# Performance work log

Hardware: AMD Instinct MI355X
Metric: run time of the kernel (lower is better)

The kernel has to match this reference:

```python
import jax, jax.numpy as jnp
from jax import lax
import numpy as np

DIM, RESO, HEADS, SPLIT, B = 128, 112, 4, 7, 2
HID = 4 * DIM  # mlp_ratio=4


def _ln(x, g, b):
    m = x.mean(-1, keepdims=True)
    v = ((x - m) ** 2).mean(-1, keepdims=True)
    return (x - m) * lax.rsqrt(v + 1e-5) * g + b


def _lepe_attn(q, k, v, cw, cb, H, W, H_sp, W_sp, nh):
    # q,k,v: [B, H*W, C] (C = branch dim); cw: depthwise conv weight [C,1,3,3]
    Bq, L, C = q.shape
    hd = C // nh
    scale = hd ** -0.5
    nHw, nWw = H // H_sp, W // W_sp

    def to_win(t):  # [B,H,W,C] -> [B*nHw*nWw, nh, H_sp*W_sp, hd]
        t = t.reshape(Bq, nHw, H_sp, nWw, W_sp, C).transpose(0, 1, 3, 2, 4, 5)
        return t.reshape(-1, H_sp * W_sp, nh, hd).transpose(0, 2, 1, 3)

    qw = to_win(q.reshape(Bq, H, W, C)) * scale
    kw = to_win(k.reshape(Bq, H, W, C))

    # v path: window partition in NCHW, depthwise conv LePE per window
    vimg = v.transpose(0, 2, 1).reshape(Bq, C, H, W)
    vimg = vimg.reshape(Bq, C, nHw, H_sp, nWw, W_sp).transpose(0, 2, 4, 1, 3, 5)
    vimg = vimg.reshape(-1, C, H_sp, W_sp)  # [B', C, H_sp, W_sp]
    lepe = lax.conv_general_dilated(vimg, cw, (1, 1), 'SAME', feature_group_count=C,
                                    dimension_numbers=('NCHW', 'OIHW', 'NCHW'))
    lepe = lepe + cb[None, :, None, None]
    vw = vimg.reshape(-1, nh, hd, H_sp * W_sp).transpose(0, 1, 3, 2)
    lepe = lepe.reshape(-1, nh, hd, H_sp * W_sp).transpose(0, 1, 3, 2)

    attn = jax.nn.softmax(jnp.einsum('whnd,whmd->whnm', qw, kw), axis=-1)
    o = jnp.einsum('whnm,whmd->whnd', attn, vw) + lepe  # [B', nh, S, hd]

    # windows2img
    o = o.transpose(0, 2, 1, 3).reshape(-1, H_sp * W_sp, C)
    o = o.reshape(Bq, nHw, nWw, H_sp, W_sp, C).transpose(0, 1, 3, 2, 4, 5)
    return o.reshape(Bq, H * W, C)


def setup_inputs() -> dict:
    key = jax.random.key(0)
    ks = jax.random.split(key, 16)
    s = 0.02
    Cb = DIM // 2
    return {
        'x': jax.random.normal(ks[0], (B, RESO * RESO, DIM), jnp.float32),
        'g1': jnp.ones((DIM,), jnp.float32),
        'b1': jnp.zeros((DIM,), jnp.float32),
        'w_qkv': s * jax.random.normal(ks[1], (3 * DIM, DIM), jnp.float32),
        'conv_w0': s * jax.random.normal(ks[2], (Cb, 1, 3, 3), jnp.float32),
        'conv_b0': jnp.zeros((Cb,), jnp.float32),
        'conv_w1': s * jax.random.normal(ks[3], (Cb, 1, 3, 3), jnp.float32),
        'conv_b1': jnp.zeros((Cb,), jnp.float32),
        'w_proj': s * jax.random.normal(ks[4], (DIM, DIM), jnp.float32),
        'b_proj': jnp.zeros((DIM,), jnp.float32),
        'g2': jnp.ones((DIM,), jnp.float32),
        'b2': jnp.zeros((DIM,), jnp.float32),
        'w_fc1': s * jax.random.normal(ks[5], (HID, DIM), jnp.float32),
        'b_fc1': jnp.zeros((HID,), jnp.float32),
        'w_fc2': s * jax.random.normal(ks[6], (DIM, HID), jnp.float32),
        'b_fc2': jnp.zeros((DIM,), jnp.float32),
    }


def reference(x, g1, b1, w_qkv, conv_w0, conv_b0, conv_w1, conv_b1,
              w_proj, b_proj, g2, b2, w_fc1, b_fc1, w_fc2, b_fc2):
    Bq, L, C = x.shape
    Cb = C // 2
    nh_b = HEADS // 2
    img = _ln(x, g1, b1)
    qkv = (img @ w_qkv.T).reshape(Bq, L, 3, C)  # qkv_bias=False
    q, k, v = qkv[:, :, 0], qkv[:, :, 1], qkv[:, :, 2]
    # branch 0: horizontal stripes (H_sp=RESO, W_sp=SPLIT) on first half of channels
    x1 = _lepe_attn(q[..., :Cb], k[..., :Cb], v[..., :Cb], conv_w0, conv_b0,
                    RESO, RESO, RESO, SPLIT, nh_b)
    # branch 1: vertical stripes (H_sp=SPLIT, W_sp=RESO) on second half
    x2 = _lepe_attn(q[..., Cb:], k[..., Cb:], v[..., Cb:], conv_w1, conv_b1,
                    RESO, RESO, SPLIT, RESO, nh_b)
    att = jnp.concatenate([x1, x2], axis=2)
    att = att @ w_proj.T + b_proj
    x = x + att  # drop_path = identity (prob 0)
    y = _ln(x, g2, b2)
    h = jax.nn.gelu(y @ w_fc1.T + b_fc1, approximate=False)
    x = x + (h @ w_fc2.T + b_fc2)
    return x
```

## Files before the change

kernel.cpp:

```cpp
#include <hip/hip_runtime.h>
#include <cstdint>

#define LTOK 12544
#define BATCH 2
#define CDIM 128
#define C3 384
#define RES 112
#define NROWS (BATCH * LTOK)
#define SCALE 0.17677669529663687f

typedef __attribute__((ext_vector_type(8))) short bf16x8;
typedef __attribute__((ext_vector_type(4))) float f32x4;

__device__ inline ushort f2b(float f) {
    union { float f; unsigned u; } v; v.f = f;
    unsigned r = (v.u + 0x7FFFu + ((v.u >> 16) & 1u)) >> 16;
    return (ushort)r;
}
__device__ inline float b2f(ushort u) {
    union { float f; unsigned u; } v; v.u = ((unsigned)u) << 16; return v.f;
}
__device__ inline float gelu_f(float a) {
    return 0.5f * a * (1.0f + erff(a * 0.70710678118654752f));
}

__device__ inline int ysIdx(int row, int el) { return row * 128 + (el ^ ((row & 7) << 3)); }
__device__ inline int hsIdx(int row, int el) { return row * 256 + (el ^ ((row & 7) << 3)); }
__device__ inline int xsIdx(int row, int el) { return row * 128 + (el ^ ((row & 7) << 2)); }

__device__ inline void nij(int n, int branch, int& i, int& j) {
    if (branch == 0) { i = n / 7; j = n - i * 7; }
    else             { i = n / 112; j = n - i * 112; }
}

__global__ __launch_bounds__(256) void k_cvt(const float* __restrict__ w0, const float* __restrict__ w1,
        const float* __restrict__ w2, const float* __restrict__ w3,
        ushort* __restrict__ o0, ushort* __restrict__ o1,
        ushort* __restrict__ o2, ushort* __restrict__ o3)
{
    int idx = blockIdx.x * 256 + threadIdx.x;
    const float* src; ushort* dst; int vi;
    if      (idx < 12288) { src = w0; dst = o0; vi = idx; }
    else if (idx < 16384) { src = w1; dst = o1; vi = idx - 12288; }
    else if (idx < 32768) { src = w2; dst = o2; vi = idx - 16384; }
    else                  { src = w3; dst = o3; vi = idx - 32768; }
    float4 v = ((const float4*)src)[vi];
    ushort4 r; r.x = f2b(v.x); r.y = f2b(v.y); r.z = f2b(v.z); r.w = f2b(v.w);
    ((ushort4*)dst)[vi] = r;
}

__global__ __launch_bounds__(256, 2) void k_ln_qkv(const float* __restrict__ x,
        const float* __restrict__ g1, const float* __restrict__ b1,
        const ushort* __restrict__ wqkv_bf, ushort* __restrict__ qkv)
{
    __shared__ ushort ys[32 * 128];
    const int tid = threadIdx.x;
    const long long row0 = (long long)blockIdx.x * 32;

    {
        const int r = tid >> 3, l8 = tid & 7;
        const float* xr = x + (row0 + r) * CDIM + l8 * 16;
        float4 a[4];
        #pragma unroll
        for (int i = 0; i < 4; ++i) a[i] = ((const float4*)xr)[i];
        float s = 0.f, s2 = 0.f;
        #pragma unroll
        for (int i = 0; i < 4; ++i) {
            s  += a[i].x + a[i].y + a[i].z + a[i].w;
            s2 += a[i].x*a[i].x + a[i].y*a[i].y + a[i].z*a[i].z + a[i].w*a[i].w;
        }
        #pragma unroll
        for (int m = 4; m >= 1; m >>= 1) { s += __shfl_xor(s, m, 8); s2 += __shfl_xor(s2, m, 8); }
        const float mean = s * (1.f / 128.f);
        const float var = s2 * (1.f / 128.f) - mean * mean;
        const float rs = rsqrtf(var + 1e-5f);
        #pragma unroll
        for (int i = 0; i < 4; ++i) {
            float4 gg = *(const float4*)(g1 + l8 * 16 + i * 4);
            float4 bb = *(const float4*)(b1 + l8 * 16 + i * 4);
            ushort4 w;
            w.x = f2b((a[i].x - mean) * rs * gg.x + bb.x);
            w.y = f2b((a[i].y - mean) * rs * gg.y + bb.y);
            w.z = f2b((a[i].z - mean) * rs * gg.z + bb.z);
            w.w = f2b((a[i].w - mean) * rs * gg.w + bb.w);
            *(ushort4*)&ys[ysIdx(r, l8 * 16 + i * 4)] = w;
        }
    }
    __syncthreads();

    const int wv = tid >> 6, lane = tid & 63;
    const int c16 = lane & 15, g = lane >> 4;

    bf16x8 yb[2][4];
    #pragma unroll
    for (int mt = 0; mt < 2; ++mt)
        #pragma unroll
        for (int kc = 0; kc < 4; ++kc)
            yb[mt][kc] = *(const bf16x8*)&ys[ysIdx(mt * 16 + c16, kc * 32 + g * 8)];

    bf16x8 wr[6][4];
    #pragma unroll
    for (int t = 0; t < 6; ++t)
        #pragma unroll
        for (int kc = 0; kc < 4; ++kc)
            wr[t][kc] = *(const bf16x8*)&wqkv_bf[(wv * 96 + t * 16 + c16) * CDIM + kc * 32 + g * 8];

    #pragma unroll
    for (int t = 0; t < 6; ++t) {
        const int n0 = wv * 96 + t * 16;
        #pragma unroll
        for (int mt = 0; mt < 2; ++mt) {
            f32x4 acc = {0.f, 0.f, 0.f, 0.f};
            #pragma unroll
            for (int kc = 0; kc < 4; ++kc)
                acc = __builtin_amdgcn_mfma_f32_16x16x32_bf16(wr[t][kc], yb[mt][kc], acc, 0, 0, 0);
            ushort4 sv;
            sv.x = f2b(acc[0]); sv.y = f2b(acc[1]); sv.z = f2b(acc[2]); sv.w = f2b(acc[3]);
            *(ushort4*)&qkv[(row0 + mt * 16 + c16) * C3 + n0 + g * 4] = sv;
        }
    }
}

__global__ __launch_bounds__(256) void k_attn_mfma(const ushort* __restrict__ qkv,
        const float* __restrict__ cw0, const float* __restrict__ cb0,
        const float* __restrict__ cw1, const float* __restrict__ cb1,
        ushort* __restrict__ att)
{
    __shared__ __align__(16) ushort ks[112 * 40];
    __shared__ __align__(16) ushort vt[32 * 136];
    __shared__ __align__(16) ushort pl[4][16 * 40];
    __shared__ __align__(16) float  ol[4][16 * 36];

    const int tid = threadIdx.x;
    const int wv = tid >> 6, lane = tid & 63;
    const int g = lane >> 4, c16 = lane & 15;

    const int wh = blockIdx.x;
    const int branch = wh >> 6;
    const int idx = wh & 63;
    const int win = idx >> 1, head = idx & 1;
    const int b = win >> 4, w = win & 15;
    const int rowBase = branch ? w * 7 : 0;
    const int colBase = branch ? 0 : w * 7;
    const float* cw = branch ? cw1 : cw0;
    const float* cb = branch ? cb1 : cb0;
    const int cbase = branch * 64 + head * 32;
    const long long qkvB = (long long)b * LTOK * C3;

    {
        const int row = tid >> 3, cwd = tid & 7;
        *(unsigned*)&vt[row * 136 + 112 + cwd * 2] = 0u;
    }

    const int t0 = blockIdx.y * 7 + 2 * wv;
    const int nt = (2 * wv + 1 < 7) ? 2 : 1;

    bf16x8 qf[2];
    #pragma unroll
    for (int t = 0; t < 2; ++t) if (t < nt) {
        int n = (t0 + t) * 16 + c16;
        int i, j; nij(n, branch, i, j);
        const ushort* qp = qkv + qkvB + (long long)((rowBase + i) * RES + colBase + j) * C3 + cbase + g * 8;
        bf16x8 qq = *(const bf16x8*)qp;
        #pragma unroll
        for (int e = 0; e < 8; ++e) qq[e] = (short)f2b(b2f((ushort)qq[e]) * SCALE);
        qf[t] = qq;
    }

    f32x4 O00 = {0.f,0.f,0.f,0.f}, O01 = {0.f,0.f,0.f,0.f};
    f32x4 O10 = {0.f,0.f,0.f,0.f}, O11 = {0.f,0.f,0.f,0.f};
    float lsum0[4] = {0.f,0.f,0.f,0.f};
    float lsum1[4] = {0.f,0.f,0.f,0.f};

    for (int cc = 0; cc < 7; ++cc) {
        __syncthreads();
        for (int u = tid; u < 448; u += 256) {
            const int key = u >> 2, d8 = (u & 3) * 8;
            const int n = cc * 112 + key;
            int i, j; nij(n, branch, i, j);
            const ushort* base = qkv + qkvB + (long long)((rowBase + i) * RES + colBase + j) * C3 + cbase + d8;
            bf16x8 kk = *(const bf16x8*)(base + 128);
            bf16x8 vv = *(const bf16x8*)(base + 256);
            *(bf16x8*)&ks[key * 40 + d8] = kk;
            #pragma unroll
            for (int e = 0; e < 8; ++e) vt[(d8 + e) * 136 + key] = (ushort)vv[e];
        }
        __syncthreads();

        #pragma unroll
        for (int p = 0; p < 4; ++p) {
            bf16x8 kf0 = *(const bf16x8*)&ks[(p * 32 + c16) * 40 + g * 8];
            bf16x8 kf1;
            if (p < 3) kf1 = *(const bf16x8*)&ks[(p * 32 + 16 + c16) * 40 + g * 8];
            bf16x8 vf0 = *(const bf16x8*)&vt[c16 * 136 + p * 32 + g * 8];
            bf16x8 vf1 = *(const bf16x8*)&vt[(16 + c16) * 136 + p * 32 + g * 8];
            ushort* pb = &pl[wv][0];

            #pragma unroll
            for (int t = 0; t < 2; ++t) if (t < nt) {
                const bf16x8 qq = t ? qf[1] : qf[0];
                f32x4 z = {0.f,0.f,0.f,0.f};
                f32x4 S0 = __builtin_amdgcn_mfma_f32_16x16x32_bf16(qq, kf0, z, 0, 0, 0);
                f32x4 S1 = z;
                if (p < 3) S1 = __builtin_amdgcn_mfma_f32_16x16x32_bf16(qq, kf1, z, 0, 0, 0);
                ushort pw0[4], pw1[4];
                #pragma unroll
                for (int r = 0; r < 4; ++r) {
                    float e0 = __expf(S0[r]);
                    if (t) lsum1[r] += e0; else lsum0[r] += e0;
                    pw0[r] = f2b(e0);
                    if (p < 3) {
                        float e1 = __expf(S1[r]);
                        if (t) lsum1[r] += e1; else lsum0[r] += e1;
                        pw1[r] = f2b(e1);
                    } else pw1[r] = 0;
                }
                #pragma unroll
                for (int r = 0; r < 4; ++r) {
                    pb[(g * 4 + r) * 40 + c16]      = pw0[r];
                    pb[(g * 4 + r) * 40 + 16 + c16] = pw1[r];
                }
                bf16x8 pf = *(const bf16x8*)&pb[c16 * 40 + g * 8];
                if (t) {
                    O10 = __builtin_amdgcn_mfma_f32_16x16x32_bf16(pf, vf0, O10, 0, 0, 0);
                    O11 = __builtin_amdgcn_mfma_f32_16x16x32_bf16(pf, vf1, O11, 0, 0, 0);
                } else {
                    O00 = __builtin_amdgcn_mfma_f32_16x16x32_bf16(pf, vf0, O00, 0, 0, 0);
                    O01 = __builtin_amdgcn_mfma_f32_16x16x32_bf16(pf, vf1, O01, 0, 0, 0);
                }
            }
        }
    }

    const int H_sp = branch ? 7 : RES;
    const int W_sp = branch ? RES : 7;
    #pragma unroll
    for (int t = 0; t < 2; ++t) if (t < nt) {
        float* ob = &ol[wv][0];
        #pragma unroll
        for (int r = 0; r < 4; ++r) {
            float s = t ? lsum1[r] : lsum0[r];
            s += __shfl_xor(s, 1); s += __shfl_xor(s, 2);
            s += __shfl_xor(s, 4); s += __shfl_xor(s, 8);
            const float inv = 1.f / s;
            const f32x4 Oa = t ? O10 : O00;
            const f32x4 Ob = t ? O11 : O01;
            ob[(g * 4 + r) * 36 + c16]      = Oa[r] * inv;
            ob[(g * 4 + r) * 36 + 16 + c16] = Ob[r] * inv;
        }
        const int r2 = lane >> 2, db = (lane & 3) * 8;
        const int n0 = (t0 + t) * 16 + r2;
        int i0, j0; nij(n0, branch, i0, j0);
        float acc[8];
        #pragma unroll
        for (int e = 0; e < 8; ++e) acc[e] = ob[r2 * 36 + db + e] + cb[head * 32 + db + e];
        #pragma unroll
        for (int dij = 0; dij < 9; ++dij) {
            const int di = dij / 3 - 1, dj = dij % 3 - 1;
            const int ii = i0 + di, jj = j0 + dj;
            if (ii >= 0 && ii < H_sp && jj >= 0 && jj < W_sp) {
                const ushort* vp = qkv + qkvB + (long long)((rowBase + ii) * RES + colBase + jj) * C3 + 256 + cbase + db;
                bf16x8 vv = *(const bf16x8*)vp;
                #pragma unroll
                for (int e = 0; e < 8; ++e)
                    acc[e] += cw[(head * 32 + db + e) * 9 + dij] * b2f((ushort)vv[e]);
            }
        }
        const long long Lq = (long long)(rowBase + i0) * RES + colBase + j0;
        ushort* op = att + ((long long)b * LTOK + Lq) * CDIM + cbase + db;
        bf16x8 ov;
        #pragma unroll
        for (int e = 0; e < 8; ++e) ov[e] = (short)f2b(acc[e]);
        *(bf16x8*)op = ov;
    }
}

__global__ __launch_bounds__(256, 2) void k_pmlp(const ushort* __restrict__ att,
        const ushort* __restrict__ wproj_bf, const float* __restrict__ bproj,
        const float* __restrict__ x,
        const float* __restrict__ g2, const float* __restrict__ b2,
        const ushort* __restrict__ w1bf, const float* __restrict__ bfc1,
        const ushort* __restrict__ w2bf, const float* __restrict__ bfc2,
        float* __restrict__ out)
{
    __shared__ union {
        float  xs[32 * 128];
        ushort hs[32 * 256];
    } u;
    __shared__ ushort ys[32 * 128];
    const int tid = threadIdx.x;
    const int wv = tid >> 6, lane = tid & 63;
    const int c16 = lane & 15, g = lane >> 4;
    const long long row0 = (long long)blockIdx.x * 32;

    f32x4 resid[2][2];
    {
        bf16x8 ab[2][4];
        #pragma unroll
        for (int mt = 0; mt < 2; ++mt)
            #pragma unroll
            for (int kc = 0; kc < 4; ++kc)
                ab[mt][kc] = *(const bf16x8*)&att[(row0 + mt * 16 + c16) * CDIM + kc * 32 + g * 8];

        bf16x8 awp[2][4];
        #pragma unroll
        for (int tt = 0; tt < 2; ++tt)
            #pragma unroll
            for (int kc = 0; kc < 4; ++kc)
                awp[tt][kc] = *(const bf16x8*)&wproj_bf[(wv * 32 + tt * 16 + c16) * CDIM + kc * 32 + g * 8];

        #pragma unroll
        for (int tt = 0; tt < 2; ++tt) {
            const int col = wv * 32 + tt * 16 + g * 4;
            float4 bb = *(const float4*)&bproj[col];
            #pragma unroll
            for (int mt = 0; mt < 2; ++mt) {
                f32x4 a = {0.f, 0.f, 0.f, 0.f};
                #pragma unroll
                for (int kc = 0; kc < 4; ++kc)
                    a = __builtin_amdgcn_mfma_f32_16x16x32_bf16(awp[tt][kc], ab[mt][kc], a, 0, 0, 0);
                float4 xv = *(const float4*)&x[(row0 + mt * 16 + c16) * CDIM + col];
                f32x4 r;
                r[0] = a[0] + xv.x + bb.x;
                r[1] = a[1] + xv.y + bb.y;
                r[2] = a[2] + xv.z + bb.z;
                r[3] = a[3] + xv.w + bb.w;
                resid[tt][mt] = r;
                *(float4*)&u.xs[xsIdx(mt * 16 + c16, col)] = make_float4(r[0], r[1], r[2], r[3]);
            }
        }
    }
    __syncthreads();

    {
        const int r = tid >> 3, l8 = tid & 7;
        float4 a[4];
        #pragma unroll
        for (int i = 0; i < 4; ++i) a[i] = *(const float4*)&u.xs[xsIdx(r, l8 * 16 + i * 4)];
        float s = 0.f, s2 = 0.f;
        #pragma unroll
        for (int i = 0; i < 4; ++i) {
            s  += a[i].x + a[i].y + a[i].z + a[i].w;
            s2 += a[i].x*a[i].x + a[i].y*a[i].y + a[i].z*a[i].z + a[i].w*a[i].w;
        }
        #pragma unroll
        for (int m = 4; m >= 1; m >>= 1) { s += __shfl_xor(s, m, 8); s2 += __shfl_xor(s2, m, 8); }
        const float mean = s * (1.f / 128.f);
        const float var = s2 * (1.f / 128.f) - mean * mean;
        const float rs = rsqrtf(var + 1e-5f);
        #pragma unroll
        for (int i = 0; i < 4; ++i) {
            float4 gg = *(const float4*)(g2 + l8 * 16 + i * 4);
            float4 bb = *(const float4*)(b2 + l8 * 16 + i * 4);
            ushort4 w;
            w.x = f2b((a[i].x - mean) * rs * gg.x + bb.x);
            w.y = f2b((a[i].y - mean) * rs * gg.y + bb.y);
            w.z = f2b((a[i].z - mean) * rs * gg.z + bb.z);
            w.w = f2b((a[i].w - mean) * rs * gg.w + bb.w);
            *(ushort4*)&ys[ysIdx(r, l8 * 16 + i * 4)] = w;
        }
    }
    __syncthreads();

    bf16x8 yb[2][4];
    #pragma unroll
    for (int mt = 0; mt < 2; ++mt)
        #pragma unroll
        for (int kc = 0; kc < 4; ++kc)
            yb[mt][kc] = *(const bf16x8*)&ys[ysIdx(mt * 16 + c16, kc * 32 + g * 8)];

    f32x4 acc2[2][2];
    #pragma unroll
    for (int tt = 0; tt < 2; ++tt)
        #pragma unroll
        for (int mt = 0; mt < 2; ++mt)
            acc2[tt][mt] = (f32x4){0.f, 0.f, 0.f, 0.f};

    #pragma unroll
    for (int half = 0; half < 2; ++half) {
        bf16x8 w1r[4][4];
        #pragma unroll
        for (int t = 0; t < 4; ++t)
            #pragma unroll
            for (int kc = 0; kc < 4; ++kc)
                w1r[t][kc] = *(const bf16x8*)&w1bf[(half * 256 + wv * 64 + t * 16 + c16) * CDIM + kc * 32 + g * 8];

        #pragma unroll
        for (int t = 0; t < 4; ++t) {
            const int n0g = half * 256 + wv * 64 + t * 16;
            float4 b1v = *(const float4*)&bfc1[n0g + g * 4];
            #pragma unroll
            for (int mt = 0; mt < 2; ++mt) {
                f32x4 a = {0.f, 0.f, 0.f, 0.f};
                #pragma unroll
                for (int kc = 0; kc < 4; ++kc)
                    a = __builtin_amdgcn_mfma_f32_16x16x32_bf16(w1r[t][kc], yb[mt][kc], a, 0, 0, 0);
                ushort4 sv;
                sv.x = f2b(gelu_f(a[0] + b1v.x));
                sv.y = f2b(gelu_f(a[1] + b1v.y));
                sv.z = f2b(gelu_f(a[2] + b1v.z));
                sv.w = f2b(gelu_f(a[3] + b1v.w));
                *(ushort4*)&u.hs[hsIdx(mt * 16 + c16, wv * 64 + t * 16 + g * 4)] = sv;
            }
        }

        bf16x8 w2r[2][8];
        #pragma unroll
        for (int tt = 0; tt < 2; ++tt)
            #pragma unroll
            for (int kc = 0; kc < 8; ++kc)
                w2r[tt][kc] = *(const bf16x8*)&w2bf[(wv * 32 + tt * 16 + c16) * 512 + half * 256 + kc * 32 + g * 8];

        __syncthreads();

        #pragma unroll
        for (int kc = 0; kc < 8; ++kc) {
            bf16x8 hb[2];
            #pragma unroll
            for (int mt = 0; mt < 2; ++mt)
                hb[mt] = *(const bf16x8*)&u.hs[hsIdx(mt * 16 + c16, kc * 32 + g * 8)];
            #pragma unroll
            for (int tt = 0; tt < 2; ++tt)
                #pragma unroll
                for (int mt = 0; mt < 2; ++mt)
                    acc2[tt][mt] = __builtin_amdgcn_mfma_f32_16x16x32_bf16(w2r[tt][kc], hb[mt], acc2[tt][mt], 0, 0, 0);
        }
        if (half == 0) __syncthreads();
    }

    #pragma unroll
    for (int tt = 0; tt < 2; ++tt) {
        const int col = wv * 32 + tt * 16 + g * 4;
        float4 bb = *(const float4*)&bfc2[col];
        #pragma unroll
        for (int mt = 0; mt < 2; ++mt) {
            const long long row = row0 + mt * 16 + c16;
            float4 o;
            o.x = acc2[tt][mt][0] + resid[tt][mt][0] + bb.x;
            o.y = acc2[tt][mt][1] + resid[tt][mt][1] + bb.y;
            o.z = acc2[tt][mt][2] + resid[tt][mt][2] + bb.z;
            o.w = acc2[tt][mt][3] + resid[tt][mt][3] + bb.w;
            *(float4*)&out[row * CDIM + col] = o;
        }
    }
}

extern "C" void kernel_launch(void* const* d_in, const int* in_sizes, int n_in,
                              void* d_out, int out_size, void* d_ws, size_t ws_size,
                              hipStream_t stream) {
    const float* x     = (const float*)d_in[0];
    const float* g1    = (const float*)d_in[1];
    const float* b1    = (const float*)d_in[2];
    const float* wqkv  = (const float*)d_in[3];
    const float* cw0   = (const float*)d_in[4];
    const float* cb0   = (const float*)d_in[5];
    const float* cw1   = (const float*)d_in[6];
    const float* cb1   = (const float*)d_in[7];
    const float* wproj = (const float*)d_in[8];
    const float* bproj = (const float*)d_in[9];
    const float* g2    = (const float*)d_in[10];
    const float* b2    = (const float*)d_in[11];
    const float* wfc1  = (const float*)d_in[12];
    const float* bfc1  = (const float*)d_in[13];
    const float* wfc2  = (const float*)d_in[14];
    const float* bfc2  = (const float*)d_in[15];

    char* wsb = (char*)d_ws;
    ushort* qkv_bf   = (ushort*)wsb;
    ushort* att_bf   = (ushort*)(wsb + 19267584);
    char*   wbase    = wsb + 19267584 + 6422528;
    ushort* wqkv_bf  = (ushort*)(wbase);
    ushort* wproj_bf = (ushort*)(wbase + 98304);
    ushort* wfc1_bf  = (ushort*)(wbase + 98304 + 32768);
    ushort* wfc2_bf  = (ushort*)(wbase + 98304 + 32768 + 131072);

    float* out = (float*)d_out;

    k_cvt<<<192, 256, 0, stream>>>(wqkv, wproj, wfc1, wfc2, wqkv_bf, wproj_bf, wfc1_bf, wfc2_bf);
    k_ln_qkv<<<NROWS / 32, 256, 0, stream>>>(x, g1, b1, wqkv_bf, qkv_bf);
    k_attn_mfma<<<dim3(128, 7), 256, 0, stream>>>(qkv_bf, cw0, cb0, cw1, cb1, att_bf);
    k_pmlp<<<NROWS / 32, 256, 0, stream>>>(att_bf, wproj_bf, bproj, x, g2, b2,
                                           wfc1_bf, bfc1, wfc2_bf, bfc2, out);
}
```

Before: 122.6 us.

## Double block size to 512 threads in LN-QKV and proj-MLP kernels

Both fused row-block kernels now run 8 waves per 32-row block instead of 4, so each wave owns half as many output columns. The LayerNorm stage uses 16 threads per row. The MLP kernel drops its two-pass split of the hidden dimension: the full 512-wide GELU hidden tile goes into shared memory and FC2 runs as a single K=512 pass. This raises parallelism per block and removes a sync round, but doubles LDS use for the hidden buffer and may lower blocks per CU and weight-register reuse per wave.

Result: slower. 135.7 us (+10.7%).

```diff
diff --git a/kernel.cpp b/kernel.cpp
--- a/kernel.cpp
+++ b/kernel.cpp
@@ -25,7 +25,7 @@
 }
 
 __device__ inline int ysIdx(int row, int el) { return row * 128 + (el ^ ((row & 7) << 3)); }
-__device__ inline int hsIdx(int row, int el) { return row * 256 + (el ^ ((row & 7) << 3)); }
+__device__ inline int hsIdx(int row, int el) { return row * 512 + (el ^ ((row & 7) << 3)); }
 __device__ inline int xsIdx(int row, int el) { return row * 128 + (el ^ ((row & 7) << 2)); }
 
 __device__ inline void nij(int n, int branch, int& i, int& j) {
@@ -49,7 +49,7 @@
     ((ushort4*)dst)[vi] = r;
 }
 
-__global__ __launch_bounds__(256, 2) void k_ln_qkv(const float* __restrict__ x,
+__global__ __launch_bounds__(512) void k_ln_qkv(const float* __restrict__ x,
         const float* __restrict__ g1, const float* __restrict__ b1,
         const ushort* __restrict__ wqkv_bf, ushort* __restrict__ qkv)
 {
@@ -58,33 +58,33 @@
     const long long row0 = (long long)blockIdx.x * 32;
 
     {
-        const int r = tid >> 3, l8 = tid & 7;
-        const float* xr = x + (row0 + r) * CDIM + l8 * 16;
-        float4 a[4];
-        #pragma unroll
-        for (int i = 0; i < 4; ++i) a[i] = ((const float4*)xr)[i];
-        float s = 0.f, s2 = 0.f;
-        #pragma unroll
-        for (int i = 0; i < 4; ++i) {
-            s  += a[i].x + a[i].y + a[i].z + a[i].w;
-            s2 += a[i].x*a[i].x + a[i].y*a[i].y + a[i].z*a[i].z + a[i].w*a[i].w;
-        }
-        #pragma unroll
-        for (int m = 4; m >= 1; m >>= 1) { s += __shfl_xor(s, m, 8); s2 += __shfl_xor(s2, m, 8); }
+        const int r = tid >> 4, l16 = tid & 15;
+        const float* xr = x + (row0 + r) * CDIM + l16 * 8;
+        float4 a0 = *(const float4*)xr;
+        float4 a1 = *(const float4*)(xr + 4);
+        float s  = a0.x + a0.y + a0.z + a0.w + a1.x + a1.y + a1.z + a1.w;
+        float s2 = a0.x*a0.x + a0.y*a0.y + a0.z*a0.z + a0.w*a0.w
+                 + a1.x*a1.x + a1.y*a1.y + a1.z*a1.z + a1.w*a1.w;
+        #pragma unroll
+        for (int m = 8; m >= 1; m >>= 1) { s += __shfl_xor(s, m, 16); s2 += __shfl_xor(s2, m, 16); }
         const float mean = s * (1.f / 128.f);
         const float var = s2 * (1.f / 128.f) - mean * mean;
         const float rs = rsqrtf(var + 1e-5f);
-        #pragma unroll
-        for (int i = 0; i < 4; ++i) {
-            float4 gg = *(const float4*)(g1 + l8 * 16 + i * 4);
-            float4 bb = *(const float4*)(b1 + l8 * 16 + i * 4);
-            ushort4 w;
-            w.x = f2b((a[i].x - mean) * rs * gg.x + bb.x);
-            w.y = f2b((a[i].y - mean) * rs * gg.y + bb.y);
-            w.z = f2b((a[i].z - mean) * rs * gg.z + bb.z);
-            w.w = f2b((a[i].w - mean) * rs * gg.w + bb.w);
-            *(ushort4*)&ys[ysIdx(r, l8 * 16 + i * 4)] = w;
-        }
+        float4 g0 = *(const float4*)(g1 + l16 * 8);
+        float4 g4 = *(const float4*)(g1 + l16 * 8 + 4);
+        float4 c0 = *(const float4*)(b1 + l16 * 8);
+        float4 c4 = *(const float4*)(b1 + l16 * 8 + 4);
+        ushort4 w0, w1;
+        w0.x = f2b((a0.x - mean) * rs * g0.x + c0.x);
+        w0.y = f2b((a0.y - mean) * rs * g0.y + c0.y);
+        w0.z = f2b((a0.z - mean) * rs * g0.z + c0.z);
+        w0.w = f2b((a0.w - mean) * rs * g0.w + c0.w);
+        w1.x = f2b((a1.x - mean) * rs * g4.x + c4.x);
+        w1.y = f2b((a1.y - mean) * rs * g4.y + c4.y);
+        w1.z = f2b((a1.z - mean) * rs * g4.z + c4.z);
+        w1.w = f2b((a1.w - mean) * rs * g4.w + c4.w);
+        *(ushort4*)&ys[ysIdx(r, l16 * 8)]     = w0;
+        *(ushort4*)&ys[ysIdx(r, l16 * 8 + 4)] = w1;
     }
     __syncthreads();
 
@@ -98,16 +98,16 @@
         for (int kc = 0; kc < 4; ++kc)
             yb[mt][kc] = *(const bf16x8*)&ys[ysIdx(mt * 16 + c16, kc * 32 + g * 8)];
 
-    bf16x8 wr[6][4];
-    #pragma unroll
-    for (int t = 0; t < 6; ++t)
+    bf16x8 wr[3][4];
+    #pragma unroll
+    for (int t = 0; t < 3; ++t)
         #pragma unroll
         for (int kc = 0; kc < 4; ++kc)
-            wr[t][kc] = *(const bf16x8*)&wqkv_bf[(wv * 96 + t * 16 + c16) * CDIM + kc * 32 + g * 8];
-
-    #pragma unroll
-    for (int t = 0; t < 6; ++t) {
-        const int n0 = wv * 96 + t * 16;
+            wr[t][kc] = *(const bf16x8*)&wqkv_bf[(wv * 48 + t * 16 + c16) * CDIM + kc * 32 + g * 8];
+
+    #pragma unroll
+    for (int t = 0; t < 3; ++t) {
+        const int n0 = wv * 48 + t * 16;
         #pragma unroll
         for (int mt = 0; mt < 2; ++mt) {
             f32x4 acc = {0.f, 0.f, 0.f, 0.f};
@@ -275,7 +275,7 @@
     }
 }
 
-__global__ __launch_bounds__(256, 2) void k_pmlp(const ushort* __restrict__ att,
+__global__ __launch_bounds__(512) void k_pmlp(const ushort* __restrict__ att,
         const ushort* __restrict__ wproj_bf, const float* __restrict__ bproj,
         const float* __restrict__ x,
         const float* __restrict__ g2, const float* __restrict__ b2,
@@ -285,7 +285,7 @@
 {
     __shared__ union {
         float  xs[32 * 128];
-        ushort hs[32 * 256];
+        ushort hs[32 * 512];
     } u;
     __shared__ ushort ys[32 * 128];
     const int tid = threadIdx.x;
@@ -293,7 +293,7 @@
     const int c16 = lane & 15, g = lane >> 4;
     const long long row0 = (long long)blockIdx.x * 32;
 
-    f32x4 resid[2][2];
+    f32x4 resid[2];
     {
         bf16x8 ab[2][4];
         #pragma unroll
@@ -302,63 +302,58 @@
             for (int kc = 0; kc < 4; ++kc)
                 ab[mt][kc] = *(const bf16x8*)&att[(row0 + mt * 16 + c16) * CDIM + kc * 32 + g * 8];
 
-        bf16x8 awp[2][4];
-        #pragma unroll
-        for (int tt = 0; tt < 2; ++tt)
+        bf16x8 awp[4];
+        #pragma unroll
+        for (int kc = 0; kc < 4; ++kc)
+            awp[kc] = *(const bf16x8*)&wproj_bf[(wv * 16 + c16) * CDIM + kc * 32 + g * 8];
+
+        const int col = wv * 16 + g * 4;
+        float4 bb = *(const float4*)&bproj[col];
+        #pragma unroll
+        for (int mt = 0; mt < 2; ++mt) {
+            f32x4 a = {0.f, 0.f, 0.f, 0.f};
             #pragma unroll
             for (int kc = 0; kc < 4; ++kc)
-                awp[tt][kc] = *(const bf16x8*)&wproj_bf[(wv * 32 + tt * 16 + c16) * CDIM + kc * 32 + g * 8];
-
-        #pragma unroll
-        for (int tt = 0; tt < 2; ++tt) {
-            const int col = wv * 32 + tt * 16 + g * 4;
-            float4 bb = *(const float4*)&bproj[col];
-            #pragma unroll
-            for (int mt = 0; mt < 2; ++mt) {
-                f32x4 a = {0.f, 0.f, 0.f, 0.f};
-                #pragma unroll
-                for (int kc = 0; kc < 4; ++kc)
-                    a = __builtin_amdgcn_mfma_f32_16x16x32_bf16(awp[tt][kc], ab[mt][kc], a, 0, 0, 0);
-                float4 xv = *(const float4*)&x[(row0 + mt * 16 + c16) * CDIM + col];
-                f32x4 r;
-                r[0] = a[0] + xv.x + bb.x;
-                r[1] = a[1] + xv.y + bb.y;
-                r[2] = a[2] + xv.z + bb.z;
-                r[3] = a[3] + xv.w + bb.w;
-                resid[tt][mt] = r;
-                *(float4*)&u.xs[xsIdx(mt * 16 + c16, col)] = make_float4(r[0], r[1], r[2], r[3]);
-            }
+                a = __builtin_amdgcn_mfma_f32_16x16x32_bf16(awp[kc], ab[mt][kc], a, 0, 0, 0);
+            float4 xv = *(const float4*)&x[(row0 + mt * 16 + c16) * CDIM + col];
+            f32x4 r;
+            r[0] = a[0] + xv.x + bb.x;
+            r[1] = a[1] + xv.y + bb.y;
+            r[2] = a[2] + xv.z + bb.z;
+            r[3] = a[3] + xv.w + bb.w;
+            resid[mt] = r;
+            *(float4*)&u.xs[xsIdx(mt * 16 + c16, col)] = make_float4(r[0], r[1], r[2], r[3]);
         }
     }
     __syncthreads();
 
     {
-        const int r = tid >> 3, l8 = tid & 7;
-        float4 a[4];
-        #pragma unroll
-        for (int i = 0; i < 4; ++i) a[i] = *(const float4*)&u.xs[xsIdx(r, l8 * 16 + i * 4)];
-        float s = 0.f, s2 = 0.f;
-        #pragma unroll
-        for (int i = 0; i < 4; ++i) {
-            s  += a[i].x + a[i].y + a[i].z + a[i].w;
-            s2 += a[i].x*a[i].x + a[i].y*a[i].y + a[i].z*a[i].z + a[i].w*a[i].w;
-        }
-        #pragma unroll
-        for (int m = 4; m >= 1; m >>= 1) { s += __shfl_xor(s, m, 8); s2 += __shfl_xor(s2, m, 8); }
+        const int r = tid >> 4, l16 = tid & 15;
+        float4 a0 = *(const float4*)&u.xs[xsIdx(r, l16 * 8)];
+        float4 a1 = *(const float4*)&u.xs[xsIdx(r, l16 * 8 + 4)];
+        float s  = a0.x + a0.y + a0.z + a0.w + a1.x + a1.y + a1.z + a1.w;
+        float s2 = a0.x*a0.x + a0.y*a0.y + a0.z*a0.z + a0.w*a0.w
+                 + a1.x*a1.x + a1.y*a1.y + a1.z*a1.z + a1.w*a1.w;
+        #pragma unroll
+        for (int m = 8; m >= 1; m >>= 1) { s += __shfl_xor(s, m, 16); s2 += __shfl_xor(s2, m, 16); }
         const float mean = s * (1.f / 128.f);
         const float var = s2 * (1.f / 128.f) - mean * mean;
         const float rs = rsqrtf(var + 1e-5f);
-        #pragma unroll
-        for (int i = 0; i < 4; ++i) {
-            float4 gg = *(const float4*)(g2 + l8 * 16 + i * 4);
-            float4 bb = *(const float4*)(b2 + l8 * 16 + i * 4);
-            ushort4 w;
-            w.x = f2b((a[i].x - mean) * rs * gg.x + bb.x);
-            w.y = f2b((a[i].y - mean) * rs * gg.y + bb.y);
-            w.z = f2b((a[i].z - mean) * rs * gg.z + bb.z);
-            w.w = f2b((a[i].w - mean) * rs * gg.w + bb.w);
-            *(ushort4*)&ys[ysIdx(r, l8 * 16 + i * 4)] = w;
-        }
+        float4 g0 = *(const float4*)(g2 + l16 * 8);
+        float4 g4 = *(const float4*)(g2 + l16 * 8 + 4);
+        float4 c0 = *(const float4*)(b2 + l16 * 8);
+        float4 c4 = *(const float4*)(b2 + l16 * 8 + 4);
+        ushort4 w0, w1;
+        w0.x = f2b((a0.x - mean) * rs * g0.x + c0.x);
+        w0.y = f2b((a0.y - mean) * rs * g0.y + c0.y);
+        w0.z = f2b((a0.z - mean) * rs * g0.z + c0.z);
+        w0.w = f2b((a0.w - mean) * rs * g0.w + c0.w);
+        w1.x = f2b((a1.x - mean) * rs * g4.x + c4.x);
+        w1.y = f2b((a1.y - mean) * rs * g4.y + c4.y);
+        w1.z = f2b((a1.z - mean) * rs * g4.z + c4.z);
+        w1.w = f2b((a1.w - mean) * rs * g4.w + c4.w);
+        *(ushort4*)&ys[ysIdx(r, l16 * 8)]     = w0;
+        *(ushort4*)&ys[ysIdx(r, l16 * 8 + 4)] = w1;
     }
     __syncthreads();
 
@@ -369,25 +364,17 @@
         for (int kc = 0; kc < 4; ++kc)
             yb[mt][kc] = *(const bf16x8*)&ys[ysIdx(mt * 16 + c16, kc * 32 + g * 8)];
 
-    f32x4 acc2[2][2];
-    #pragma unroll
-    for (int tt = 0; tt < 2; ++tt)
-        #pragma unroll
-        for (int mt = 0; mt < 2; ++mt)
-            acc2[tt][mt] = (f32x4){0.f, 0.f, 0.f, 0.f};
-
-    #pragma unroll
-    for (int half = 0; half < 2; ++half) {
+    {
         bf16x8 w1r[4][4];
         #pragma unroll
         for (int t = 0; t < 4; ++t)
             #pragma unroll
             for (int kc = 0; kc < 4; ++kc)
-                w1r[t][kc] = *(const bf16x8*)&w1bf[(half * 256 + wv * 64 + t * 16 + c16) * CDIM + kc * 32 + g * 8];
+                w1r[t][kc] = *(const bf16x8*)&w1bf[(wv * 64 + t * 16 + c16) * CDIM + kc * 32 + g * 8];
 
         #pragma unroll
         for (int t = 0; t < 4; ++t) {
-            const int n0g = half * 256 + wv * 64 + t * 16;
+            const int n0g = wv * 64 + t * 16;
             float4 b1v = *(const float4*)&bfc1[n0g + g * 4];
             #pragma unroll
             for (int mt = 0; mt < 2; ++mt) {
@@ -400,46 +387,41 @@
                 sv.y = f2b(gelu_f(a[1] + b1v.y));
                 sv.z = f2b(gelu_f(a[2] + b1v.z));
                 sv.w = f2b(gelu_f(a[3] + b1v.w));
-                *(ushort4*)&u.hs[hsIdx(mt * 16 + c16, wv * 64 + t * 16 + g * 4)] = sv;
+                *(ushort4*)&u.hs[hsIdx(mt * 16 + c16, n0g + g * 4)] = sv;
             }
         }
-
-        bf16x8 w2r[2][8];
-        #pragma unroll
-        for (int tt = 0; tt < 2; ++tt)
-            #pragma unroll
-            for (int kc = 0; kc < 8; ++kc)
-                w2r[tt][kc] = *(const bf16x8*)&w2bf[(wv * 32 + tt * 16 + c16) * 512 + half * 256 + kc * 32 + g * 8];
-
-        __syncthreads();
-
-        #pragma unroll
-        for (int kc = 0; kc < 8; ++kc) {
-            bf16x8 hb[2];
-            #pragma unroll
-            for (int mt = 0; mt < 2; ++mt)
-                hb[mt] = *(const bf16x8*)&u.hs[hsIdx(mt * 16 + c16, kc * 32 + g * 8)];
-            #pragma unroll
-            for (int tt = 0; tt < 2; ++tt)
-                #pragma unroll
-                for (int mt = 0; mt < 2; ++mt)
-                    acc2[tt][mt] = __builtin_amdgcn_mfma_f32_16x16x32_bf16(w2r[tt][kc], hb[mt], acc2[tt][mt], 0, 0, 0);
-        }
-        if (half == 0) __syncthreads();
-    }
-
-    #pragma unroll
-    for (int tt = 0; tt < 2; ++tt) {
-        const int col = wv * 32 + tt * 16 + g * 4;
+    }
+
+    bf16x8 w2r[16];
+    #pragma unroll
+    for (int kc = 0; kc < 16; ++kc)
+        w2r[kc] = *(const bf16x8*)&w2bf[(wv * 16 + c16) * 512 + kc * 32 + g * 8];
+
+    __syncthreads();
+
+    f32x4 acc2[2] = {{0.f,0.f,0.f,0.f},{0.f,0.f,0.f,0.f}};
+    #pragma unroll
+    for (int kc = 0; kc < 16; ++kc) {
+        bf16x8 hb[2];
+        #pragma unroll
+        for (int mt = 0; mt < 2; ++mt)
+            hb[mt] = *(const bf16x8*)&u.hs[hsIdx(mt * 16 + c16, kc * 32 + g * 8)];
+        #pragma unroll
+        for (int mt = 0; mt < 2; ++mt)
+            acc2[mt] = __builtin_amdgcn_mfma_f32_16x16x32_bf16(w2r[kc], hb[mt], acc2[mt], 0, 0, 0);
+    }
+
+    {
+        const int col = wv * 16 + g * 4;
         float4 bb = *(const float4*)&bfc2[col];
         #pragma unroll
         for (int mt = 0; mt < 2; ++mt) {
             const long long row = row0 + mt * 16 + c16;
             float4 o;
-            o.x = acc2[tt][mt][0] + resid[tt][mt][0] + bb.x;
-            o.y = acc2[tt][mt][1] + resid[tt][mt][1] + bb.y;
-            o.z = acc2[tt][mt][2] + resid[tt][mt][2] + bb.z;
-            o.w = acc2[tt][mt][3] + resid[tt][mt][3] + bb.w;
+            o.x = acc2[mt][0] + resid[mt][0] + bb.x;
+            o.y = acc2[mt][1] + resid[mt][1] + bb.y;
+            o.z = acc2[mt][2] + resid[mt][2] + bb.z;
+            o.w = acc2[mt][3] + resid[mt][3] + bb.w;
             *(float4*)&out[row * CDIM + col] = o;
         }
     }
@@ -477,8 +459,8 @@
     float* out = (float*)d_out;
 
     k_cvt<<<192, 256, 0, stream>>>(wqkv, wproj, wfc1, wfc2, wqkv_bf, wproj_bf, wfc1_bf, wfc2_bf);
-    k_ln_qkv<<<NROWS / 32, 256, 0, stream>>>(x, g1, b1, wqkv_bf, qkv_bf);
+    k_ln_qkv<<<NROWS / 32, 512, 0, stream>>>(x, g1, b1, wqkv_bf, qkv_bf);
     k_attn_mfma<<<dim3(128, 7), 256, 0, stream>>>(qkv_bf, cw0, cb0, cw1, cb1, att_bf);
-    k_pmlp<<<NROWS / 32, 256, 0, stream>>>(att_bf, wproj_bf, bproj, x, g2, b2,
+    k_pmlp<<<NROWS / 32, 512, 0, stream>>>(att_bf, wproj_bf, bproj, x, g2, b2,
                                            wfc1_bf, bfc1, wfc2_bf, bfc2, out);
 }
```
